# Optimization experiments

Measured on AMD Instinct MI355X. Metric: run time of the kernel, lower is better.

The kernel has to match this reference:

```python
import jax, jax.numpy as jnp
import numpy as np

DET_SIZE = 5120
DET_THRESHOLD = 0.5
NMS_THRESHOLD = 0.4
STRIDES = (8, 16, 32)
NUM_ANCHORS = 2
TOP_K = 2048  # fixed pre-NMS candidate count (jit-friendly stand-in for torch.where filtering)


def _anchor_centers(stride):
    n = DET_SIZE // stride
    g = jnp.arange(n, dtype=jnp.float32) * stride
    X, Y = jnp.meshgrid(g, g, indexing='xy')       # matches torch.meshgrid(..., indexing='xy')
    c = jnp.stack([X, Y], axis=-1).reshape(-1, 2)  # (n*n, 2), x fastest
    return jnp.repeat(c, NUM_ANCHORS, axis=0)      # stack([c]*2, dim=1).reshape(-1,2) == interleaved repeat


def _pairwise_iou(b):
    # b: (K,4) xyxy
    area = jnp.clip(b[:, 2] - b[:, 0], 0.0) * jnp.clip(b[:, 3] - b[:, 1], 0.0)
    lt = jnp.maximum(b[:, None, :2], b[None, :, :2])
    rb = jnp.minimum(b[:, None, 2:], b[None, :, 2:])
    wh = jnp.clip(rb - lt, 0.0)
    inter = wh[..., 0] * wh[..., 1]
    return inter / (area[:, None] + area[None, :] - inter + 1e-9)


def _forward(scores8, bbox8, lms8, scores16, bbox16, lms16, scores32, bbox32, lms32, det_scale):
    confs, boxes, lmss = [], [], []
    per_stride = [(scores8, bbox8, lms8), (scores16, bbox16, lms16), (scores32, bbox32, lms32)]
    for (conf, bbox, lms), stride in zip(per_stride, STRIDES):
        c = _anchor_centers(stride)                 # (N,2)
        b = bbox * stride                            # distance-style offsets scaled by stride
        l = lms * stride
        box = jnp.concatenate([c - b[:, :2], c + b[:, 2:4]], axis=-1) / det_scale  # (N,4) xyxy
        pts = (c[:, None, :] + l.reshape(-1, 5, 2)) / det_scale                    # (N,5,2)
        confs.append(conf.reshape(-1)); boxes.append(box); lmss.append(pts)
    conf = jnp.concatenate(confs)
    box = jnp.concatenate(boxes, axis=0)
    pts = jnp.concatenate(lmss, axis=0)
    # score threshold via masking (fixed shapes); below-threshold entries get conf=-1
    conf_m = jnp.where(conf >= DET_THRESHOLD, conf, -1.0)
    top_conf, top_idx = jax.lax.top_k(conf_m, TOP_K)
    top_box = box[top_idx]          # (K,4)
    top_pts = pts[top_idx]          # (K,5,2)
    valid = top_conf >= DET_THRESHOLD
    iou = _pairwise_iou(top_box)    # (K,K)
    later = jnp.arange(TOP_K)
    def body(i, keep):
        supp = (iou[i] > NMS_THRESHOLD) & (later > i) & keep[i] & valid[i]
        return keep & ~supp
    keep = jax.lax.fori_loop(0, TOP_K, body, valid)  # greedy NMS in descending-score order
    m = keep.astype(top_box.dtype)
    # (K, 15) = [conf | bbox(4) | lms(10)], suppressed/invalid rows zeroed
    return jnp.concatenate([(top_conf * m)[:, None], top_box * m[:, None], top_pts.reshape(TOP_K, 10) * m[:, None]], axis=-1)


def setup_inputs() -> dict:
    key = jax.random.key(0)
    ks = jax.random.split(key, 9)
    inp = {}
    for i, s in enumerate(STRIDES):
        n = DET_SIZE // s
        N = n * n * NUM_ANCHORS
        inp[f'scores{s}'] = jax.random.uniform(ks[3 * i], (N,), dtype=jnp.float32)
        inp[f'bbox{s}'] = jax.random.uniform(ks[3 * i + 1], (N, 4), dtype=jnp.float32) * 8.0
        inp[f'lms{s}'] = jax.random.normal(ks[3 * i + 2], (N, 10), dtype=jnp.float32) * 4.0
    inp['det_scale'] = jnp.array(0.5, dtype=jnp.float32)
    return inp


def reference(scores8, bbox8, lms8, scores16, bbox16, lms16, scores32, bbox32, lms32, det_scale):
    return _forward(scores8, bbox8, lms8, scores16, bbox16, lms16, scores32, bbox32, lms32, det_scale)
```

## Files before the change

### kernel.cpp

```cpp
#include <hip/hip_runtime.h>
#include <stdint.h>
#include <stddef.h>

#pragma clang fp contract(off)

#define N8   819200u
#define N16  204800u
#define N32  51200u
#define NTOT 1075200u
#define TOPK 2048
#define CAND_MAX 8192
#define NBIN 16384u
#define BINSHIFT 9
#define NMS_THR 0.4f
#define DET_THR 0.5f

#define OFF_HIST   0u
#define OFF_META   65536u
#define OFF_CAND   65600u
#define OFF_TIDX   131136u
#define OFF_TCONF  139328u
#define OFF_BOX    147520u
#define OFF_KEEP   180544u
#define OFF_SUPP   180800u

__device__ __forceinline__ float load_conf(unsigned a, const float* __restrict__ s8,
                                           const float* __restrict__ s16,
                                           const float* __restrict__ s32) {
  if (a < N8) return s8[a];
  if (a < N8 + N16) return s16[a - N8];
  return s32[a - (N8 + N16)];
}

__device__ __forceinline__ void decode(unsigned a,
    const float* __restrict__ b8, const float* __restrict__ l8,
    const float* __restrict__ b16, const float* __restrict__ l16,
    const float* __restrict__ b32, const float* __restrict__ l32,
    float& cx, float& cy, float& s, const float*& bb, const float*& lm) {
  if (a < N8) {
    unsigned cell = a >> 1;
    cx = (float)((cell % 640u) * 8u); cy = (float)((cell / 640u) * 8u);
    s = 8.f; bb = b8 + (size_t)a * 4; lm = l8 + (size_t)a * 10;
  } else if (a < N8 + N16) {
    unsigned loc = a - N8; unsigned cell = loc >> 1;
    cx = (float)((cell % 320u) * 16u); cy = (float)((cell / 320u) * 16u);
    s = 16.f; bb = b16 + (size_t)loc * 4; lm = l16 + (size_t)loc * 10;
  } else {
    unsigned loc = a - (N8 + N16); unsigned cell = loc >> 1;
    cx = (float)((cell % 160u) * 32u); cy = (float)((cell / 160u) * 32u);
    s = 32.f; bb = b32 + (size_t)loc * 4; lm = l32 + (size_t)loc * 10;
  }
}

__global__ void k_hist(const float* __restrict__ s8, const float* __restrict__ s16,
                       const float* __restrict__ s32, unsigned* __restrict__ hist) {
  unsigned i = blockIdx.x * blockDim.x + threadIdx.x;
  unsigned st = gridDim.x * blockDim.x;
  for (unsigned a = i; a < NTOT; a += st) {
    float c = load_conf(a, s8, s16, s32);
    if (c >= DET_THR) {
      unsigned v = (__float_as_uint(c) - 0x3F000000u) >> BINSHIFT;
      if (v > NBIN - 1u) v = NBIN - 1u;
      atomicAdd(&hist[v], 1u);
    }
  }
}

__global__ void __launch_bounds__(1024) k_scan(const unsigned* __restrict__ hist,
                                               unsigned* __restrict__ meta) {
  __shared__ unsigned suf[1024];
  int t = threadIdx.x;
  const unsigned* hp = hist + (size_t)t * 16;
  unsigned s = 0;
  for (int b = 0; b < 16; b++) s += hp[b];
  suf[t] = s;
  __syncthreads();
  for (int d = 1; d < 1024; d <<= 1) {
    unsigned v = (t + d < 1024) ? suf[t + d] : 0u;
    __syncthreads();
    suf[t] += v;
    __syncthreads();
  }
  unsigned total = suf[0];
  unsigned mine = suf[t];
  unsigned nxt = (t < 1023) ? suf[t + 1] : 0u;
  if (total < (unsigned)TOPK) {
    if (t == 0) { meta[0] = 0u; meta[2] = total; }
    return;
  }
  if (mine >= (unsigned)TOPK && nxt < (unsigned)TOPK) {
    unsigned run = nxt, cut = (unsigned)t * 16u;
    for (int b = 15; b >= 0; b--) {
      run += hp[b];
      if (run >= (unsigned)TOPK) { cut = (unsigned)t * 16u + (unsigned)b; break; }
    }
    meta[0] = cut; meta[2] = total;
  }
}

__global__ void k_compact(const float* __restrict__ s8, const float* __restrict__ s16,
                          const float* __restrict__ s32, unsigned* __restrict__ meta,
                          unsigned long long* __restrict__ cand) {
  unsigned cut = meta[0];
  unsigned i = blockIdx.x * blockDim.x + threadIdx.x;
  unsigned st = gridDim.x * blockDim.x;
  for (unsigned a = i; a < NTOT; a += st) {
    float c = load_conf(a, s8, s16, s32);
    if (c >= DET_THR) {
      unsigned b = __float_as_uint(c);
      unsigned v = (b - 0x3F000000u) >> BINSHIFT;
      if (v >= cut) {
        unsigned pos = atomicAdd(&meta[3], 1u);
        if (pos < (unsigned)CAND_MAX)
          cand[pos] = ((unsigned long long)b << 32) |
                      (unsigned long long)(0xFFFFFFFFu - a);
      }
    }
  }
}

__global__ void __launch_bounds__(256) k_rank(
    const unsigned long long* __restrict__ cand, const unsigned* __restrict__ meta,
    const float* __restrict__ b8, const float* __restrict__ l8,
    const float* __restrict__ b16, const float* __restrict__ l16,
    const float* __restrict__ b32, const float* __restrict__ l32,
    const float* __restrict__ dsp,
    unsigned* __restrict__ tidx, float* __restrict__ tconf, float* __restrict__ box) {
  unsigned count = meta[3];
  if (count > (unsigned)CAND_MAX) count = (unsigned)CAND_MAX;
  unsigned wave = blockIdx.x * 4u + (threadIdx.x >> 6);
  unsigned lane = threadIdx.x & 63u;
  if (wave >= count) return;
  unsigned long long my = cand[wave];
  unsigned cnt = 0;
  for (unsigned i = lane; i < count; i += 64u)
    cnt += (cand[i] > my) ? 1u : 0u;
  for (int d = 32; d > 0; d >>= 1) cnt += __shfl_down(cnt, d);
  if (lane == 0 && cnt < (unsigned)TOPK) {
    unsigned r = cnt;
    unsigned a = 0xFFFFFFFFu - (unsigned)(my & 0xFFFFFFFFull);
    float conf = __uint_as_float((unsigned)(my >> 32));
    float cx, cy, s; const float* bb; const float* lm;
    decode(a, b8, l8, b16, l16, b32, l32, cx, cy, s, bb, lm);
    float ds = dsp[0];
    float b0 = bb[0] * s, b1 = bb[1] * s, b2 = bb[2] * s, b3 = bb[3] * s;
    box[r * 4 + 0] = (cx - b0) / ds;
    box[r * 4 + 1] = (cy - b1) / ds;
    box[r * 4 + 2] = (cx + b2) / ds;
    box[r * 4 + 3] = (cy + b3) / ds;
    tidx[r] = a; tconf[r] = conf;
  }
}

__global__ void __launch_bounds__(256) k_supp(const float* __restrict__ box,
                                              unsigned long long* __restrict__ supp) {
  int i = blockIdx.x;
  const float4 bi = ((const float4*)box)[i];
  float ai = fmaxf(bi.z - bi.x, 0.f) * fmaxf(bi.w - bi.y, 0.f);
  int tid = threadIdx.x;
  int lane = tid & 63, wv = tid >> 6;
  for (int base = 0; base < TOPK; base += 256) {
    int j = base + tid;
    const float4 bj = ((const float4*)box)[j];
    float aj = fmaxf(bj.z - bj.x, 0.f) * fmaxf(bj.w - bj.y, 0.f);
    float ltx = fmaxf(bi.x, bj.x), lty = fmaxf(bi.y, bj.y);
    float rbx = fminf(bi.z, bj.z), rby = fminf(bi.w, bj.w);
    float w = fmaxf(rbx - ltx, 0.f), h = fmaxf(rby - lty, 0.f);
    float inter = w * h;
    float iou = inter / (ai + aj - inter + 1e-9f);
    bool pred = (iou > NMS_THR) && (j > i);
    unsigned long long word = __ballot(pred);
    if (lane == 0) supp[(size_t)i * 32 + (base >> 6) + wv] = word;
  }
}

__global__ void __launch_bounds__(64) k_nms(const unsigned* __restrict__ supp32,
                                            const unsigned* __restrict__ meta,
                                            unsigned* __restrict__ keepmask) {
  int lane = threadIdx.x;
  unsigned count = meta[3];
  if (count > (unsigned)TOPK) count = (unsigned)TOPK;
  unsigned lo = (unsigned)lane * 32u;
  unsigned kw = (count >= lo + 32u) ? 0xFFFFFFFFu
              : (count <= lo ? 0u : ((1u << (count - lo)) - 1u));
  const unsigned* sp = supp32 + lane;
  unsigned Ta[32], Tb[32];
#define LOADT(BUF, C)                                                         \
  _Pragma("unroll") for (int k = 0; k < 32; k++)                              \
      BUF[k] = sp[((size_t)((C) * 32 + k)) * 64];
#define PROCESS(BUF, C)                                                       \
  {                                                                           \
    unsigned w = __builtin_amdgcn_readlane(kw, (C));                          \
    _Pragma("unroll") for (int k = 0; k < 32; k++) {                          \
      unsigned mk = 0u - ((w >> k) & 1u);                                     \
      w &= ~(BUF[k] & mk);                                                    \
    }                                                                         \
    w = __builtin_amdgcn_readlane(w, (C));                                    \
    unsigned acc = 0u;                                                        \
    _Pragma("unroll") for (int k = 0; k < 32; k++) {                          \
      unsigned mk = 0u - ((w >> k) & 1u);                                     \
      acc |= BUF[k] & mk;                                                     \
    }                                                                         \
    kw &= ~acc;                                                               \
  }
  LOADT(Ta, 0)
#pragma unroll 1
  for (int c = 0; c < 64; c += 2) {
    LOADT(Tb, c + 1)
    PROCESS(Ta, c)
    if (c + 2 < 64) LOADT(Ta, c + 2)
    PROCESS(Tb, c + 1)
  }
#undef LOADT
#undef PROCESS
  keepmask[lane] = kw;
}

__global__ void __launch_bounds__(256) k_out(
    const unsigned* __restrict__ keepmask,
    const unsigned* __restrict__ tidx, const float* __restrict__ tconf,
    const float* __restrict__ b8, const float* __restrict__ l8,
    const float* __restrict__ b16, const float* __restrict__ l16,
    const float* __restrict__ b32, const float* __restrict__ l32,
    const float* __restrict__ dsp, float* __restrict__ out) {
  int r = blockIdx.x * 256 + threadIdx.x;
  if (r >= TOPK) return;
  bool kept = (keepmask[r >> 5] >> (r & 31)) & 1u;
  float o[15];
  if (kept) {
    unsigned a = tidx[r];
    float cx, cy, s; const float* bb; const float* lm;
    decode(a, b8, l8, b16, l16, b32, l32, cx, cy, s, bb, lm);
    float ds = dsp[0];
    o[0] = tconf[r];
    float b0 = bb[0] * s, b1 = bb[1] * s, b2 = bb[2] * s, b3 = bb[3] * s;
    o[1] = (cx - b0) / ds;
    o[2] = (cy - b1) / ds;
    o[3] = (cx + b2) / ds;
    o[4] = (cy + b3) / ds;
    for (int p = 0; p < 5; p++) {
      float lx = lm[2 * p] * s, ly = lm[2 * p + 1] * s;
      o[5 + 2 * p] = (cx + lx) / ds;
      o[6 + 2 * p] = (cy + ly) / ds;
    }
  } else {
    for (int c = 0; c < 15; c++) o[c] = 0.f;
  }
  for (int c = 0; c < 15; c++) out[(size_t)r * 15 + c] = o[c];
}

extern "C" void kernel_launch(void* const* d_in, const int* in_sizes, int n_in,
                              void* d_out, int out_size, void* d_ws, size_t ws_size,
                              hipStream_t stream) {
  const float* s8  = (const float*)d_in[0];
  const float* b8  = (const float*)d_in[1];
  const float* l8  = (const float*)d_in[2];
  const float* s16 = (const float*)d_in[3];
  const float* b16 = (const float*)d_in[4];
  const float* l16 = (const float*)d_in[5];
  const float* s32 = (const float*)d_in[6];
  const float* b32 = (const float*)d_in[7];
  const float* l32 = (const float*)d_in[8];
  const float* dsp = (const float*)d_in[9];
  char* ws = (char*)d_ws;
  unsigned* hist = (unsigned*)(ws + OFF_HIST);
  unsigned* meta = (unsigned*)(ws + OFF_META);
  unsigned long long* cand = (unsigned long long*)(ws + OFF_CAND);
  unsigned* tidx = (unsigned*)(ws + OFF_TIDX);
  float* tconf = (float*)(ws + OFF_TCONF);
  float* box = (float*)(ws + OFF_BOX);
  unsigned* keepm = (unsigned*)(ws + OFF_KEEP);
  unsigned long long* supp = (unsigned long long*)(ws + OFF_SUPP);
  float* out = (float*)d_out;

  hipMemsetAsync(ws, 0, OFF_META + 64, stream);
  k_hist<<<2048, 256, 0, stream>>>(s8, s16, s32, hist);
  k_scan<<<1, 1024, 0, stream>>>(hist, meta);
  k_compact<<<2048, 256, 0, stream>>>(s8, s16, s32, meta, cand);
  k_rank<<<CAND_MAX / 4, 256, 0, stream>>>(cand, meta, b8, l8, b16, l16, b32, l32,
                                           dsp, tidx, tconf, box);
  k_supp<<<TOPK, 256, 0, stream>>>(box, supp);
  k_nms<<<1, 64, 0, stream>>>((const unsigned*)supp, meta, keepm);
  k_out<<<8, 256, 0, stream>>>(keepm, tidx, tconf, b8, l8, b16, l16, b32, l32,
                               dsp, out);
}
```

Before: 122.3 us.

## Add diagonal suppression words and deepen prefetch in serial NMS kernel

k_supp now also writes a compact diagonal array holding, for each box, the 32-bit suppression word covering its own chunk. k_nms resolves each chunk's intra-chunk dependencies from this uniform diagonal data instead of per-lane buffer values followed by a readlane. It also keeps four chunk tiles in flight instead of two, so the single-wave serial loop waits less on memory latency. The cost is more registers in a one-wave kernel and an extra global write from k_supp.

```diff
diff --git a/kernel.cpp b/kernel.cpp
--- a/kernel.cpp
+++ b/kernel.cpp
@@ -22,7 +22,8 @@
 #define OFF_TCONF  139328u
 #define OFF_BOX    147520u
 #define OFF_KEEP   180544u
-#define OFF_SUPP   180800u
+#define OFF_DIAG   180800u
+#define OFF_SUPP   188992u
 
 __device__ __forceinline__ float load_conf(unsigned a, const float* __restrict__ s8,
                                            const float* __restrict__ s16,
@@ -153,7 +154,8 @@
 }
 
 __global__ void __launch_bounds__(256) k_supp(const float* __restrict__ box,
-                                              unsigned long long* __restrict__ supp) {
+                                              unsigned long long* __restrict__ supp,
+                                              unsigned* __restrict__ diag32) {
   int i = blockIdx.x;
   const float4 bi = ((const float4*)box)[i];
   float ai = fmaxf(bi.z - bi.x, 0.f) * fmaxf(bi.w - bi.y, 0.f);
@@ -170,11 +172,17 @@
     float iou = inter / (ai + aj - inter + 1e-9f);
     bool pred = (iou > NMS_THR) && (j > i);
     unsigned long long word = __ballot(pred);
-    if (lane == 0) supp[(size_t)i * 32 + (base >> 6) + wv] = word;
+    int w64 = (base >> 6) + wv;
+    if (lane == 0) {
+      supp[(size_t)i * 32 + w64] = word;
+      if (w64 == (i >> 6))
+        diag32[i] = (unsigned)(word >> (((i >> 5) & 1) * 32));
+    }
   }
 }
 
 __global__ void __launch_bounds__(64) k_nms(const unsigned* __restrict__ supp32,
+                                            const unsigned* __restrict__ diag32,
                                             const unsigned* __restrict__ meta,
                                             unsigned* __restrict__ keepmask) {
   int lane = threadIdx.x;
@@ -184,35 +192,50 @@
   unsigned kw = (count >= lo + 32u) ? 0xFFFFFFFFu
               : (count <= lo ? 0u : ((1u << (count - lo)) - 1u));
   const unsigned* sp = supp32 + lane;
-  unsigned Ta[32], Tb[32];
+  unsigned T0[32], T1[32], T2[32], T3[32];
+  unsigned dga[32], dgb[32];
+
 #define LOADT(BUF, C)                                                         \
   _Pragma("unroll") for (int k = 0; k < 32; k++)                              \
-      BUF[k] = sp[((size_t)((C) * 32 + k)) * 64];
-#define PROCESS(BUF, C)                                                       \
+      BUF[k] = sp[((size_t)(unsigned)((C) * 32 + k)) * 64];
+#define LOADD(DBUF, C)                                                        \
+  _Pragma("unroll") for (int k = 0; k < 32; k++)                              \
+      DBUF[k] = diag32[(unsigned)((C) * 32 + k)];
+
+  LOADT(T0, 0) LOADT(T1, 1) LOADT(T2, 2) LOADT(T3, 3)
+  LOADD(dga, 0)
+
+#define STEP(BUF, DCUR, DNXT, C)                                              \
   {                                                                           \
     unsigned w = __builtin_amdgcn_readlane(kw, (C));                          \
     _Pragma("unroll") for (int k = 0; k < 32; k++) {                          \
-      unsigned mk = 0u - ((w >> k) & 1u);                                     \
-      w &= ~(BUF[k] & mk);                                                    \
+      unsigned t = ((w >> k) & 1u) ? DCUR[k] : 0u;                            \
+      w &= ~t;                                                                \
     }                                                                         \
-    w = __builtin_amdgcn_readlane(w, (C));                                    \
+    if ((C) + 1 < 64) { LOADD(DNXT, (C) + 1) }                                \
     unsigned acc = 0u;                                                        \
     _Pragma("unroll") for (int k = 0; k < 32; k++) {                          \
-      unsigned mk = 0u - ((w >> k) & 1u);                                     \
+      unsigned mk = (unsigned)((int)(w << (31 - k)) >> 31);                   \
       acc |= BUF[k] & mk;                                                     \
     }                                                                         \
     kw &= ~acc;                                                               \
-  }
-  LOADT(Ta, 0)
+    if ((C) + 4 < 64) { LOADT(BUF, (C) + 4) }                                 \
+  }
+
 #pragma unroll 1
-  for (int c = 0; c < 64; c += 2) {
-    LOADT(Tb, c + 1)
-    PROCESS(Ta, c)
-    if (c + 2 < 64) LOADT(Ta, c + 2)
-    PROCESS(Tb, c + 1)
+  for (int c = 0; c < 64; c += 8) {
+    STEP(T0, dga, dgb, c + 0)
+    STEP(T1, dgb, dga, c + 1)
+    STEP(T2, dga, dgb, c + 2)
+    STEP(T3, dgb, dga, c + 3)
+    STEP(T0, dga, dgb, c + 4)
+    STEP(T1, dgb, dga, c + 5)
+    STEP(T2, dga, dgb, c + 6)
+    STEP(T3, dgb, dga, c + 7)
   }
 #undef LOADT
-#undef PROCESS
+#undef LOADD
+#undef STEP
   keepmask[lane] = kw;
 }
 
@@ -270,6 +293,7 @@
   float* tconf = (float*)(ws + OFF_TCONF);
   float* box = (float*)(ws + OFF_BOX);
   unsigned* keepm = (unsigned*)(ws + OFF_KEEP);
+  unsigned* diag = (unsigned*)(ws + OFF_DIAG);
   unsigned long long* supp = (unsigned long long*)(ws + OFF_SUPP);
   float* out = (float*)d_out;
 
@@ -279,8 +303,8 @@
   k_compact<<<2048, 256, 0, stream>>>(s8, s16, s32, meta, cand);
   k_rank<<<CAND_MAX / 4, 256, 0, stream>>>(cand, meta, b8, l8, b16, l16, b32, l32,
                                            dsp, tidx, tconf, box);
-  k_supp<<<TOPK, 256, 0, stream>>>(box, supp);
-  k_nms<<<1, 64, 0, stream>>>((const unsigned*)supp, meta, keepm);
+  k_supp<<<TOPK, 256, 0, stream>>>(box, supp, diag);
+  k_nms<<<1, 64, 0, stream>>>((const unsigned*)supp, diag, meta, keepm);
   k_out<<<8, 256, 0, stream>>>(keepm, tidx, tconf, b8, l8, b16, l16, b32, l32,
                                dsp, out);
 }
```

New measurement: 119.9 us. About the same (-1.9%).
